# Kernel tuning notes

Hardware: AMD Instinct MI355X
Metric: run time of the kernel (lower is better)

## Reference

```python
import jax, jax.numpy as jnp
import numpy as np

B, T, D = 2, 2048, 1024
H, DH = 16, 64          # num_heads, size_per_head
NU = H * DH             # num_units == 1024


def setup_inputs() -> dict:
    key = jax.random.key(0)
    ks = jax.random.split(key, 8)
    s = 0.02
    return {
        "queries": jax.random.normal(ks[0], (B, T, D), jnp.float32),
        "keys": jax.random.normal(ks[1], (B, T, D), jnp.float32),
        "Wq": jax.random.normal(ks[2], (D, NU), jnp.float32) * s,
        "bq": jnp.zeros((NU,), jnp.float32),
        "Wk": jax.random.normal(ks[3], (D, NU), jnp.float32) * s,
        "bk": jnp.zeros((NU,), jnp.float32),
        "Wv": jax.random.normal(ks[4], (D, NU), jnp.float32) * s,
        "bv": jnp.zeros((NU,), jnp.float32),
    }


def reference(queries, keys, Wq, bq, Wk, bk, Wv, bv):
    # QKV projections
    q = queries @ Wq + bq            # [B, T, NU]
    k = keys @ Wk + bk
    v = keys @ Wv + bv
    # split heads: [B, T, H, DH] -> [B, H, T, DH]
    q_ = q.reshape(B, T, H, DH).transpose(0, 2, 1, 3)
    k_ = k.reshape(B, T, H, DH).transpose(0, 2, 1, 3)
    v_ = v.reshape(B, T, H, DH).transpose(0, 2, 1, 3)
    # scores scaled by num_units**-0.5 (full hidden dim, as in source)
    scores = jnp.einsum("bhqd,bhkd->bhqk", q_, k_) * (NU ** -0.5)
    # causal mask: triu(ones).T == lower-triangular; zeros -> -inf
    causal = jnp.tril(jnp.ones((T, T), bool))
    scores = jnp.where(causal, scores, -jnp.inf)
    weights = jax.nn.softmax(scores, axis=-1)   # [B, H, T, T]
    # dropout is identity in eval/reference
    out = jnp.einsum("bhqk,bhkd->bhqd", weights, v_)  # [B, H, T, DH]
    # merge heads back to [B, T, NU]
    out = out.transpose(0, 2, 1, 3).reshape(B, T, NU)
    return out, weights
```

## Files before the change

### kernel.cpp

```cpp
#include <hip/hip_runtime.h>
#include <cstddef>
#include <cstdint>

namespace {
constexpr int B_ = 2, T_ = 2048, D_ = 1024, H_ = 16, DH_ = 64, NU_ = 1024;
constexpr float SCALE = 0.03125f;
constexpr size_t OUT_ELEMS = (size_t)B_ * T_ * NU_;
}

using f4  = __attribute__((ext_vector_type(4))) float;
using s8v = __attribute__((ext_vector_type(8))) short;
using s4v = __attribute__((ext_vector_type(4))) short;

#define MFMA16(a, b, c) __builtin_amdgcn_mfma_f32_16x16x32_bf16((a), (b), (c), 0, 0, 0)

__device__ __forceinline__ float4 ld4(const float* p) { return *reinterpret_cast<const float4*>(p); }
__device__ __forceinline__ void st4(float* p, const float4 v) { *reinterpret_cast<float4*>(p) = v; }
__device__ __forceinline__ short f2bf(float f) {
    union { float f; uint32_t u; } v{f};
    uint32_t r = (v.u + 0x7fffu + ((v.u >> 16) & 1u)) >> 16;
    return (short)r;
}

#if __has_builtin(__builtin_amdgcn_global_load_lds)
#define HAVE_GLOAD_LDS 1
__device__ __forceinline__ void load_lds16(const void* g, void* l) {
    __builtin_amdgcn_global_load_lds(
        (const __attribute__((address_space(1))) void*)g,
        (__attribute__((address_space(3))) void*)l, 16, 0, 0);
}
#else
#define HAVE_GLOAD_LDS 0
#endif

__global__ __launch_bounds__(256) void cvt_x_kernel(
    const float* __restrict__ q, const float* __restrict__ k,
    short* __restrict__ qx, short* __restrict__ kx)
{
    const float* src = blockIdx.y ? k : q;
    short* dst       = blockIdx.y ? kx : qx;
    size_t i = ((size_t)blockIdx.x * 256 + threadIdx.x) * 8;
    float4 a = ld4(src + i), b = ld4(src + i + 4);
    s8v o = { f2bf(a.x), f2bf(a.y), f2bf(a.z), f2bf(a.w),
              f2bf(b.x), f2bf(b.y), f2bf(b.z), f2bf(b.w) };
    *reinterpret_cast<s8v*>(dst + i) = o;
}

__global__ __launch_bounds__(256) void cvt_w_kernel(
    const float* __restrict__ Wq, const float* __restrict__ Wk,
    const float* __restrict__ Wv, short* __restrict__ wt3)
{
    const int z = blockIdx.z;
    const float* W = (z == 0) ? Wq : (z == 1) ? Wk : Wv;
    short* dst = wt3 + (size_t)z * D_ * NU_;
    const int n0 = blockIdx.x * 64, k0 = blockIdx.y * 64;
    __shared__ float tl[64][68];
    const int rr = threadIdx.x >> 2, cc = (threadIdx.x & 3) * 16;
    const float* s = W + (size_t)(k0 + rr) * NU_ + n0 + cc;
    st4(&tl[rr][cc + 0],  ld4(s + 0));
    st4(&tl[rr][cc + 4],  ld4(s + 4));
    st4(&tl[rr][cc + 8],  ld4(s + 8));
    st4(&tl[rr][cc + 12], ld4(s + 12));
    __syncthreads();
    short* d = dst + (size_t)(n0 + rr) * D_ + k0 + cc;
#pragma unroll
    for (int c = 0; c < 4; ++c) {
        s4v o = { f2bf(tl[cc + c * 4 + 0][rr]), f2bf(tl[cc + c * 4 + 1][rr]),
                  f2bf(tl[cc + c * 4 + 2][rr]), f2bf(tl[cc + c * 4 + 3][rr]) };
        *reinterpret_cast<s4v*>(d + c * 4) = o;
    }
}

__global__ __launch_bounds__(256) void proj_mfma(
    const short* __restrict__ qx, const short* __restrict__ kx,
    const short* __restrict__ wt3,
    const float* __restrict__ bq, const float* __restrict__ bk,
    const float* __restrict__ bv,
    short* __restrict__ qb, short* __restrict__ kb, short* __restrict__ vt)
{
    const int lin = blockIdx.z * 256 + blockIdx.y * 8 + blockIdx.x;
    const int virt = (lin & 7) * 96 + (lin >> 3);
    const int z = virt >> 8, rem = virt & 255;
    const int m0 = (rem >> 3) * 128, n0 = (rem & 7) * 128;

    const short* __restrict__ X  = (z == 0) ? qx : kx;
    const short* __restrict__ Wt = wt3 + (size_t)z * D_ * NU_;
    const float* __restrict__ bias = (z == 0) ? bq : (z == 1) ? bk : bv;

    const int t = threadIdx.x, w = t >> 6, l = t & 63;
    const int lr = l & 15, lg = l >> 4;
    const int wr = w >> 1, wc = w & 1;

    __shared__ short Asl[128 * 64];
    __shared__ short Bsl[128 * 64];

    f4 acc[4][4];
#pragma unroll
    for (int m = 0; m < 4; ++m)
#pragma unroll
        for (int n = 0; n < 4; ++n) acc[m][n] = (f4){0.f, 0.f, 0.f, 0.f};

    for (int k0 = 0; k0 < D_; k0 += 64) {
#if HAVE_GLOAD_LDS
#pragma unroll
        for (int j = 0; j < 4; ++j) {
            const int c0 = (w * 4 + j) * 64;
            const int c  = c0 + l;
            const int row = c >> 3, qo = (c & 7) * 8;
            load_lds16(X  + (size_t)(m0 + row) * D_ + k0 + qo, (char*)Asl + (size_t)c0 * 16);
            load_lds16(Wt + (size_t)(n0 + row) * D_ + k0 + qo, (char*)Bsl + (size_t)c0 * 16);
        }
        __syncthreads();
#else
        {
            const int sr = t >> 1, sc = (t & 1) * 32;
            s8v a0 = *reinterpret_cast<const s8v*>(X  + (size_t)(m0 + sr) * D_ + k0 + sc);
            s8v a1 = *reinterpret_cast<const s8v*>(X  + (size_t)(m0 + sr) * D_ + k0 + sc + 8);
            s8v a2 = *reinterpret_cast<const s8v*>(X  + (size_t)(m0 + sr) * D_ + k0 + sc + 16);
            s8v a3 = *reinterpret_cast<const s8v*>(X  + (size_t)(m0 + sr) * D_ + k0 + sc + 24);
            s8v b0 = *reinterpret_cast<const s8v*>(Wt + (size_t)(n0 + sr) * D_ + k0 + sc);
            s8v b1 = *reinterpret_cast<const s8v*>(Wt + (size_t)(n0 + sr) * D_ + k0 + sc + 8);
            s8v b2 = *reinterpret_cast<const s8v*>(Wt + (size_t)(n0 + sr) * D_ + k0 + sc + 16);
            s8v b3 = *reinterpret_cast<const s8v*>(Wt + (size_t)(n0 + sr) * D_ + k0 + sc + 24);
            __syncthreads();
            *reinterpret_cast<s8v*>(&Asl[sr * 64 + sc])      = a0;
            *reinterpret_cast<s8v*>(&Asl[sr * 64 + sc + 8])  = a1;
            *reinterpret_cast<s8v*>(&Asl[sr * 64 + sc + 16]) = a2;
            *reinterpret_cast<s8v*>(&Asl[sr * 64 + sc + 24]) = a3;
            *reinterpret_cast<s8v*>(&Bsl[sr * 64 + sc])      = b0;
            *reinterpret_cast<s8v*>(&Bsl[sr * 64 + sc + 8])  = b1;
            *reinterpret_cast<s8v*>(&Bsl[sr * 64 + sc + 16]) = b2;
            *reinterpret_cast<s8v*>(&Bsl[sr * 64 + sc + 24]) = b3;
            __syncthreads();
        }
#endif

#pragma unroll
        for (int kk = 0; kk < 2; ++kk) {
            s8v af[4], bf[4];
#pragma unroll
            for (int m = 0; m < 4; ++m)
                af[m] = *reinterpret_cast<const s8v*>(
                    &Asl[(wr * 64 + m * 16 + lr) * 64 + kk * 32 + lg * 8]);
#pragma unroll
            for (int n = 0; n < 4; ++n)
                bf[n] = *reinterpret_cast<const s8v*>(
                    &Bsl[(wc * 64 + n * 16 + lr) * 64 + kk * 32 + lg * 8]);
#pragma unroll
            for (int m = 0; m < 4; ++m)
#pragma unroll
                for (int n = 0; n < 4; ++n)
                    acc[m][n] = MFMA16(af[m], bf[n], acc[m][n]);
        }
        __syncthreads();
    }

    if (z < 2) {
        short* __restrict__ Y = (z == 0) ? qb : kb;
#pragma unroll
        for (int n = 0; n < 4; ++n) {
            const int col = n0 + wc * 64 + n * 16 + lr;
            const float bval = bias[col];
#pragma unroll
            for (int m = 0; m < 4; ++m) {
                const int row0 = m0 + wr * 64 + m * 16 + lg * 4;
#pragma unroll
                for (int r = 0; r < 4; ++r)
                    Y[(size_t)(row0 + r) * NU_ + col] = f2bf(acc[m][n][r] + bval);
            }
        }
    } else {
#pragma unroll
        for (int n = 0; n < 4; ++n) {
            const int col = n0 + wc * 64 + n * 16 + lr;
            const float bval = bias[col];
            const int hh = col >> 6, dd = col & 63;
#pragma unroll
            for (int m = 0; m < 4; ++m) {
                const int Mi = m0 + wr * 64 + m * 16 + lg * 4;
                const int bb = Mi >> 11, t0 = Mi & 2047;
                s4v o = { f2bf(acc[m][n][0] + bval), f2bf(acc[m][n][1] + bval),
                          f2bf(acc[m][n][2] + bval), f2bf(acc[m][n][3] + bval) };
                *reinterpret_cast<s4v*>(vt + ((size_t)(bb * 16 + hh) * 64 + dd) * T_ + t0) = o;
            }
        }
    }
}

__global__ __launch_bounds__(256) void attn_pv_mfma(
    const short* __restrict__ qb, const short* __restrict__ kb,
    const short* __restrict__ vt, float* __restrict__ rsws,
    float* __restrict__ out)
{
    const int lin = blockIdx.x;
    const int xcd = lin & 7, v = lin >> 3;
    const int bh  = xcd * 4 + (v >> 5);
    const int g64 = 31 - (v & 31);
    const int b = bh >> 4, h = bh & 15;
    const int r0 = g64 * 64;
    const int t = threadIdx.x, w = t >> 6, l = t & 63;
    const int lr = l & 15, lg = l >> 4;
    const int tile16 = g64;

    __shared__ __align__(16) char smem[32 * 1024 + 1024];
    short* Pl    = (short*)smem;
    float* OA    = (float*)smem;
    float* rsbuf = (float*)(smem + 32 * 1024);

    const short* qrow0 = qb + (size_t)(b * T_ + r0 + lr) * NU_ + h * DH_ + lg * 8;
    s8v qf[4][2];
#pragma unroll
    for (int d = 0; d < 4; ++d) {
        qf[d][0] = *reinterpret_cast<const s8v*>(qrow0 + (size_t)d * 16 * NU_);
        qf[d][1] = *reinterpret_cast<const s8v*>(qrow0 + (size_t)d * 16 * NU_ + 32);
    }

    f4 acc[4][4];
#pragma unroll
    for (int d = 0; d < 4; ++d)
#pragma unroll
        for (int nt = 0; nt < 4; ++nt) acc[d][nt] = (f4){0.f, 0.f, 0.f, 0.f};
    float rsum[4] = {0.f, 0.f, 0.f, 0.f};
    const f4 zf = (f4){0.f, 0.f, 0.f, 0.f};
    const int sw = (lr & 7) << 3;
    const short* kbase0 = kb + (size_t)(b * T_) * NU_ + h * DH_ + lg * 8;
    short* PlW[4];
#pragma unroll
    for (int d = 0; d < 4; ++d) PlW[d] = &Pl[d * 4096 + w * 1024 + lr * 64];

    for (int ch = w; ch <= tile16; ch += 4) {
        const int jc = ch * 64;
        const bool diag = (ch == tile16);
        const short* kbase = kbase0 + (size_t)jc * NU_;

#pragma unroll
        for (int nt = 0; nt < 4; ++nt) {
            const short* kr = kbase + (size_t)(nt * 16 + lr) * NU_;
            s8v kf0 = *reinterpret_cast<const s8v*>(kr);
            s8v kf1 = *reinterpret_cast<const s8v*>(kr + 32);
            const int jl = nt * 16 + lg * 4;
#pragma unroll
            for (int d = 0; d < 4; ++d) {
                f4 a = MFMA16(kf0, qf[d][0], zf);
                f4 s = MFMA16(kf1, qf[d][1], a);
                float e[4];
#pragma unroll
                for (int r = 0; r < 4; ++r) {
                    float vv = __expf(s[r] * SCALE);
                    if (diag && (jl + r > d * 16 + lr)) vv = 0.f;
                    e[r] = vv;
                }
                rsum[d] += (e[0] + e[1]) + (e[2] + e[3]);
                s4v pv = { f2bf(e[0]), f2bf(e[1]), f2bf(e[2]), f2bf(e[3]) };
                *reinterpret_cast<s4v*>(PlW[d] + (jl ^ sw)) = pv;
            }
        }

        s8v pf[4][2];
#pragma unroll
        for (int d = 0; d < 4; ++d) {
            pf[d][0] = *reinterpret_cast<const s8v*>(PlW[d] + ((lg * 8) ^ sw));
            pf[d][1] = *reinterpret_cast<const s8v*>(PlW[d] + ((32 + lg * 8) ^ sw));
        }
#pragma unroll
        for (int nt = 0; nt < 4; ++nt) {
            const short* vr = vt + (size_t)(bh * 64 + nt * 16 + lr) * T_ + jc + lg * 8;
            s8v vf0 = *reinterpret_cast<const s8v*>(vr);
            s8v vf1 = *reinterpret_cast<const s8v*>(vr + 32);
#pragma unroll
            for (int d = 0; d < 4; ++d) {
                acc[d][nt] = MFMA16(pf[d][0], vf0, acc[d][nt]);
                acc[d][nt] = MFMA16(pf[d][1], vf1, acc[d][nt]);
            }
        }
    }

#pragma unroll
    for (int d = 0; d < 4; ++d) {
        rsum[d] += __shfl_xor(rsum[d], 16);
        rsum[d] += __shfl_xor(rsum[d], 32);
    }

    __syncthreads();
    if (lg == 0) {
#pragma unroll
        for (int d = 0; d < 4; ++d) rsbuf[d * 64 + w * 16 + lr] = rsum[d];
    }

#pragma unroll
    for (int d = 0; d < 4; ++d) {
#pragma unroll
        for (int nt = 0; nt < 4; ++nt)
            st4(&OA[(size_t)(w * 64 + l) * 16 + nt * 4], *(const float4*)&acc[d][nt]);
        __syncthreads();
        float osum[4] = {0.f, 0.f, 0.f, 0.f};
#pragma unroll
        for (int wv = 0; wv < 4; ++wv) {
            float4 p = *(const float4*)&OA[(size_t)(wv * 64 + l) * 16 + w * 4];
#pragma unroll
            for (int r = 0; r < 4; ++r) osum[r] += (&p.x)[r];
        }
#pragma unroll
        for (int r = 0; r < 4; ++r) {
            const int ro = lg * 4 + r;
            const float rt = rsbuf[d * 64 + ro] + rsbuf[d * 64 + 16 + ro]
                           + rsbuf[d * 64 + 32 + ro] + rsbuf[d * 64 + 48 + ro];
            out[(size_t)(b * T_ + r0 + d * 16 + ro) * NU_ + h * DH_ + w * 16 + lr] =
                osum[r] / rt;
        }
        if (w == 0 && t < 16)
            rsws[(size_t)bh * T_ + r0 + d * 16 + t] =
                rsbuf[d * 64 + t] + rsbuf[d * 64 + 16 + t]
                + rsbuf[d * 64 + 32 + t] + rsbuf[d * 64 + 48 + t];
        __syncthreads();
    }
}

__global__ __launch_bounds__(256) void attn_wts_mfma(
    const short* __restrict__ qb, const short* __restrict__ kb,
    const float* __restrict__ rsws, float* __restrict__ wts)
{
    const int lin = blockIdx.x;
    const int xcd = lin & 7, v = lin >> 3;
    const int bh  = xcd * 4 + (v >> 7);
    const int rem = v & 127;
    const int qt2 = 15 - (rem >> 3);
    const int jb  = rem & 7;
    const int b = bh >> 4, h = bh & 15;
    const int r0 = qt2 * 128;
    const int chmax = 2 * qt2 + 1;
    const int t = threadIdx.x, w = t >> 6, l = t & 63;
    const int lr = l & 15, lg = l >> 4;

    const int iA = r0 + w * 16 + lr;
    const int iB = iA + 64;

    const short* qrowA = qb + (size_t)(b * T_ + iA) * NU_ + h * DH_ + lg * 8;
    const s8v qA0 = *reinterpret_cast<const s8v*>(qrowA);
    const s8v qA1 = *reinterpret_cast<const s8v*>(qrowA + 32);
    const s8v qB0 = *reinterpret_cast<const s8v*>(qrowA + 64 * NU_);
    const s8v qB1 = *reinterpret_cast<const s8v*>(qrowA + 64 * NU_ + 32);
    const f4 zf = (f4){0.f, 0.f, 0.f, 0.f};

    const float invA = 1.f / rsws[(size_t)bh * T_ + iA];
    const float invB = 1.f / rsws[(size_t)bh * T_ + iB];
    float* const wrowA = &wts[((size_t)bh * T_ + iA) * T_];
    float* const wrowB = &wts[((size_t)bh * T_ + iB) * T_];
    const short* kbase0 = kb + (size_t)(b * T_) * NU_ + h * DH_ + lg * 8;

#pragma unroll
    for (int cx = 0; cx < 4; ++cx) {
        const int ch = jb * 4 + cx;
        const int jc = ch * 64;
        if (ch <= chmax) {
            const short* kbase = kbase0 + (size_t)jc * NU_;
            f4 sA[4], sB[4];
#pragma unroll
            for (int nt = 0; nt < 4; ++nt) {
                const short* kr = kbase + (size_t)(nt * 16 + lr) * NU_;
                s8v kf0 = *reinterpret_cast<const s8v*>(kr);
                s8v kf1 = *reinterpret_cast<const s8v*>(kr + 32);
                f4 aA = MFMA16(kf0, qA0, zf);
                sA[nt] = MFMA16(kf1, qA1, aA);
                f4 aB = MFMA16(kf0, qB0, zf);
                sB[nt] = MFMA16(kf1, qB1, aB);
            }
#pragma unroll
            for (int nt = 0; nt < 4; ++nt) {
                float4 oA, oB;
                float* eA = &oA.x;
                float* eB = &oB.x;
#pragma unroll
                for (int r = 0; r < 4; ++r) {
                    const int j = jc + nt * 16 + lg * 4 + r;
                    eA[r] = (j <= iA) ? __expf(sA[nt][r] * SCALE) * invA : 0.f;
                    eB[r] = (j <= iB) ? __expf(sB[nt][r] * SCALE) * invB : 0.f;
                }
                st4(wrowA + jc + nt * 16 + lg * 4, oA);
                st4(wrowB + jc + nt * 16 + lg * 4, oB);
            }
        } else {
            const float4 z4 = make_float4(0.f, 0.f, 0.f, 0.f);
#pragma unroll
            for (int half = 0; half < 2; ++half) {
                float* dst = &wts[((size_t)bh * T_ + r0 + half * 64 + (t >> 2)) * T_
                                  + jc + (t & 3) * 16];
                st4(dst + 0, z4); st4(dst + 4, z4);
                st4(dst + 8, z4); st4(dst + 12, z4);
            }
        }
    }
}

extern "C" void kernel_launch(void* const* d_in, const int* in_sizes, int n_in,
                              void* d_out, int out_size, void* d_ws, size_t ws_size,
                              hipStream_t stream)
{
    const float* queries = (const float*)d_in[0];
    const float* keys    = (const float*)d_in[1];
    const float* Wq = (const float*)d_in[2];
    const float* bq = (const float*)d_in[3];
    const float* Wk = (const float*)d_in[4];
    const float* bk = (const float*)d_in[5];
    const float* Wv = (const float*)d_in[6];
    const float* bv = (const float*)d_in[7];

    float* out = (float*)d_out;
    float* wts = out + OUT_ELEMS;

    short* qx = (short*)d_ws;
    short* kx = qx + (size_t)B_ * T_ * D_;
    short* wt = kx + (size_t)B_ * T_ * D_;
    short* qb = wt + (size_t)3 * D_ * NU_;
    short* kb = qb + (size_t)B_ * T_ * NU_;
    short* vt = kb + (size_t)B_ * T_ * NU_;
    float* rsws = (float*)(vt + (size_t)B_ * T_ * NU_);

    cvt_x_kernel<<<dim3((B_ * T_ * D_) / 2048, 2), 256, 0, stream>>>(queries, keys, qx, kx);
    cvt_w_kernel<<<dim3(16, 16, 3), 256, 0, stream>>>(Wq, Wk, Wv, wt);
    proj_mfma<<<dim3(8, 32, 3), 256, 0, stream>>>(
        qx, kx, wt, bq, bk, bv, qb, kb, vt);
    attn_pv_mfma<<<dim3(1024), 256, 0, stream>>>(qb, kb, vt, rsws, out);
    attn_wts_mfma<<<dim3(4096), 256, 0, stream>>>(qb, kb, rsws, wts);
}
```

Baseline: 283.8 us.

## Fuse attention weights output into PV kernel, dropping separate weights kernel

```diff
diff --git a/kernel.cpp b/kernel.cpp
--- a/kernel.cpp
+++ b/kernel.cpp
@@ -187,10 +187,10 @@
     }
 }
 
-__global__ __launch_bounds__(256) void attn_pv_mfma(
+__global__ __launch_bounds__(256) void attn_fused_mfma(
     const short* __restrict__ qb, const short* __restrict__ kb,
-    const short* __restrict__ vt, float* __restrict__ rsws,
-    float* __restrict__ out)
+    const short* __restrict__ vt, float* __restrict__ out,
+    float* __restrict__ wts)
 {
     const int lin = blockIdx.x;
     const int xcd = lin & 7, v = lin >> 3;
@@ -308,85 +308,49 @@
             out[(size_t)(b * T_ + r0 + d * 16 + ro) * NU_ + h * DH_ + w * 16 + lr] =
                 osum[r] / rt;
         }
-        if (w == 0 && t < 16)
-            rsws[(size_t)bh * T_ + r0 + d * 16 + t] =
-                rsbuf[d * 64 + t] + rsbuf[d * 64 + 16 + t]
-                + rsbuf[d * 64 + 32 + t] + rsbuf[d * 64 + 48 + t];
         __syncthreads();
     }
-}
-
-__global__ __launch_bounds__(256) void attn_wts_mfma(
-    const short* __restrict__ qb, const short* __restrict__ kb,
-    const float* __restrict__ rsws, float* __restrict__ wts)
-{
-    const int lin = blockIdx.x;
-    const int xcd = lin & 7, v = lin >> 3;
-    const int bh  = xcd * 4 + (v >> 7);
-    const int rem = v & 127;
-    const int qt2 = 15 - (rem >> 3);
-    const int jb  = rem & 7;
-    const int b = bh >> 4, h = bh & 15;
-    const int r0 = qt2 * 128;
-    const int chmax = 2 * qt2 + 1;
-    const int t = threadIdx.x, w = t >> 6, l = t & 63;
-    const int lr = l & 15, lg = l >> 4;
-
-    const int iA = r0 + w * 16 + lr;
-    const int iB = iA + 64;
-
-    const short* qrowA = qb + (size_t)(b * T_ + iA) * NU_ + h * DH_ + lg * 8;
-    const s8v qA0 = *reinterpret_cast<const s8v*>(qrowA);
-    const s8v qA1 = *reinterpret_cast<const s8v*>(qrowA + 32);
-    const s8v qB0 = *reinterpret_cast<const s8v*>(qrowA + 64 * NU_);
-    const s8v qB1 = *reinterpret_cast<const s8v*>(qrowA + 64 * NU_ + 32);
-    const f4 zf = (f4){0.f, 0.f, 0.f, 0.f};
-
-    const float invA = 1.f / rsws[(size_t)bh * T_ + iA];
-    const float invB = 1.f / rsws[(size_t)bh * T_ + iB];
-    float* const wrowA = &wts[((size_t)bh * T_ + iA) * T_];
-    float* const wrowB = &wts[((size_t)bh * T_ + iB) * T_];
-    const short* kbase0 = kb + (size_t)(b * T_) * NU_ + h * DH_ + lg * 8;
-
-#pragma unroll
-    for (int cx = 0; cx < 4; ++cx) {
-        const int ch = jb * 4 + cx;
+
+    float invd[4];
+#pragma unroll
+    for (int d = 0; d < 4; ++d)
+        invd[d] = 1.f / (rsbuf[d * 64 + lr] + rsbuf[d * 64 + 16 + lr]
+                       + rsbuf[d * 64 + 32 + lr] + rsbuf[d * 64 + 48 + lr]);
+    float* const wbase = &wts[((size_t)bh * T_ + r0 + lr) * T_];
+
+    for (int ch = w; ch < T_ / 64; ch += 4) {
         const int jc = ch * 64;
-        if (ch <= chmax) {
+        if (ch <= tile16) {
+            const bool diag = (ch == tile16);
             const short* kbase = kbase0 + (size_t)jc * NU_;
-            f4 sA[4], sB[4];
 #pragma unroll
             for (int nt = 0; nt < 4; ++nt) {
                 const short* kr = kbase + (size_t)(nt * 16 + lr) * NU_;
                 s8v kf0 = *reinterpret_cast<const s8v*>(kr);
                 s8v kf1 = *reinterpret_cast<const s8v*>(kr + 32);
-                f4 aA = MFMA16(kf0, qA0, zf);
-                sA[nt] = MFMA16(kf1, qA1, aA);
-                f4 aB = MFMA16(kf0, qB0, zf);
-                sB[nt] = MFMA16(kf1, qB1, aB);
-            }
-#pragma unroll
-            for (int nt = 0; nt < 4; ++nt) {
-                float4 oA, oB;
-                float* eA = &oA.x;
-                float* eB = &oB.x;
-#pragma unroll
-                for (int r = 0; r < 4; ++r) {
-                    const int j = jc + nt * 16 + lg * 4 + r;
-                    eA[r] = (j <= iA) ? __expf(sA[nt][r] * SCALE) * invA : 0.f;
-                    eB[r] = (j <= iB) ? __expf(sB[nt][r] * SCALE) * invB : 0.f;
+                const int jl = nt * 16 + lg * 4;
+#pragma unroll
+                for (int d = 0; d < 4; ++d) {
+                    f4 a = MFMA16(kf0, qf[d][0], zf);
+                    f4 s = MFMA16(kf1, qf[d][1], a);
+                    float4 o;
+#pragma unroll
+                    for (int r = 0; r < 4; ++r) {
+                        float vv = __expf(s[r] * SCALE) * invd[d];
+                        if (diag && (jl + r > d * 16 + lr)) vv = 0.f;
+                        (&o.x)[r] = vv;
+                    }
+                    st4(wbase + (size_t)d * 16 * T_ + jc + jl, o);
                 }
-                st4(wrowA + jc + nt * 16 + lg * 4, oA);
-                st4(wrowB + jc + nt * 16 + lg * 4, oB);
             }
         } else {
             const float4 z4 = make_float4(0.f, 0.f, 0.f, 0.f);
 #pragma unroll
-            for (int half = 0; half < 2; ++half) {
-                float* dst = &wts[((size_t)bh * T_ + r0 + half * 64 + (t >> 2)) * T_
-                                  + jc + (t & 3) * 16];
-                st4(dst + 0, z4); st4(dst + 4, z4);
-                st4(dst + 8, z4); st4(dst + 12, z4);
+            for (int nt = 0; nt < 4; ++nt) {
+                const int jl = nt * 16 + lg * 4;
+#pragma unroll
+                for (int d = 0; d < 4; ++d)
+                    st4(wbase + (size_t)d * 16 * T_ + jc + jl, z4);
             }
         }
     }
@@ -414,12 +378,10 @@
     short* qb = wt + (size_t)3 * D_ * NU_;
     short* kb = qb + (size_t)B_ * T_ * NU_;
     short* vt = kb + (size_t)B_ * T_ * NU_;
-    float* rsws = (float*)(vt + (size_t)B_ * T_ * NU_);
 
     cvt_x_kernel<<<dim3((B_ * T_ * D_) / 2048, 2), 256, 0, stream>>>(queries, keys, qx, kx);
     cvt_w_kernel<<<dim3(16, 16, 3), 256, 0, stream>>>(Wq, Wk, Wv, wt);
     proj_mfma<<<dim3(8, 32, 3), 256, 0, stream>>>(
         qx, kx, wt, bq, bk, bv, qb, kb, vt);
-    attn_pv_mfma<<<dim3(1024), 256, 0, stream>>>(qb, kb, vt, rsws, out);
-    attn_wts_mfma<<<dim3(4096), 256, 0, stream>>>(qb, kb, rsws, wts);
-}
+    attn_fused_mfma<<<dim3(1024), 256, 0, stream>>>(qb, kb, vt, out, wts);
+}
```

New measurement: 284.4 us. Within noise of the previous version (+0.2%).

## Move masked-region zero fill of weights into projection kernel launch

Applied to the files above, without the earlier changes.

```diff
diff --git a/kernel.cpp b/kernel.cpp
--- a/kernel.cpp
+++ b/kernel.cpp
@@ -76,9 +76,40 @@
     const short* __restrict__ wt3,
     const float* __restrict__ bq, const float* __restrict__ bk,
     const float* __restrict__ bv,
-    short* __restrict__ qb, short* __restrict__ kb, short* __restrict__ vt)
-{
-    const int lin = blockIdx.z * 256 + blockIdx.y * 8 + blockIdx.x;
+    short* __restrict__ qb, short* __restrict__ kb, short* __restrict__ vt,
+    float* __restrict__ wts)
+{
+    const int bid = blockIdx.x;
+    const int t = threadIdx.x, w = t >> 6, l = t & 63;
+
+    if (bid >= 768) {
+        const int f = bid - 768;
+        const int xcd = f & 7, v = f >> 3;
+        const int bh  = xcd * 4 + (v >> 7);
+        const int rem = v & 127;
+        const int qt2 = 15 - (rem >> 3);
+        const int jb  = rem & 7;
+        const int r0 = qt2 * 128;
+        const int chmax = 2 * qt2 + 1;
+        const float4 z4 = make_float4(0.f, 0.f, 0.f, 0.f);
+#pragma unroll
+        for (int cx = 0; cx < 4; ++cx) {
+            const int ch = jb * 4 + cx;
+            if (ch > chmax) {
+                const int jc = ch * 64;
+#pragma unroll
+                for (int half = 0; half < 2; ++half) {
+                    float* dst = &wts[((size_t)bh * T_ + r0 + half * 64 + (t >> 2)) * T_
+                                      + jc + (t & 3) * 16];
+                    st4(dst + 0, z4); st4(dst + 4, z4);
+                    st4(dst + 8, z4); st4(dst + 12, z4);
+                }
+            }
+        }
+        return;
+    }
+
+    const int lin = bid;
     const int virt = (lin & 7) * 96 + (lin >> 3);
     const int z = virt >> 8, rem = virt & 255;
     const int m0 = (rem >> 3) * 128, n0 = (rem & 7) * 128;
@@ -87,7 +118,6 @@
     const short* __restrict__ Wt = wt3 + (size_t)z * D_ * NU_;
     const float* __restrict__ bias = (z == 0) ? bq : (z == 1) ? bk : bv;
 
-    const int t = threadIdx.x, w = t >> 6, l = t & 63;
     const int lr = l & 15, lg = l >> 4;
     const int wr = w >> 1, wc = w & 1;
 
@@ -326,9 +356,10 @@
     const int rem = v & 127;
     const int qt2 = 15 - (rem >> 3);
     const int jb  = rem & 7;
+    const int chmax = 2 * qt2 + 1;
+    if (jb * 4 > chmax) return;
     const int b = bh >> 4, h = bh & 15;
     const int r0 = qt2 * 128;
-    const int chmax = 2 * qt2 + 1;
     const int t = threadIdx.x, w = t >> 6, l = t & 63;
     const int lr = l & 15, lg = l >> 4;
 
@@ -351,43 +382,33 @@
 #pragma unroll
     for (int cx = 0; cx < 4; ++cx) {
         const int ch = jb * 4 + cx;
+        if (ch > chmax) continue;
         const int jc = ch * 64;
-        if (ch <= chmax) {
-            const short* kbase = kbase0 + (size_t)jc * NU_;
-            f4 sA[4], sB[4];
-#pragma unroll
-            for (int nt = 0; nt < 4; ++nt) {
-                const short* kr = kbase + (size_t)(nt * 16 + lr) * NU_;
-                s8v kf0 = *reinterpret_cast<const s8v*>(kr);
-                s8v kf1 = *reinterpret_cast<const s8v*>(kr + 32);
-                f4 aA = MFMA16(kf0, qA0, zf);
-                sA[nt] = MFMA16(kf1, qA1, aA);
-                f4 aB = MFMA16(kf0, qB0, zf);
-                sB[nt] = MFMA16(kf1, qB1, aB);
-            }
-#pragma unroll
-            for (int nt = 0; nt < 4; ++nt) {
-                float4 oA, oB;
-                float* eA = &oA.x;
-                float* eB = &oB.x;
-#pragma unroll
-                for (int r = 0; r < 4; ++r) {
-                    const int j = jc + nt * 16 + lg * 4 + r;
-                    eA[r] = (j <= iA) ? __expf(sA[nt][r] * SCALE) * invA : 0.f;
-                    eB[r] = (j <= iB) ? __expf(sB[nt][r] * SCALE) * invB : 0.f;
-                }
-                st4(wrowA + jc + nt * 16 + lg * 4, oA);
-                st4(wrowB + jc + nt * 16 + lg * 4, oB);
-            }
-        } else {
-            const float4 z4 = make_float4(0.f, 0.f, 0.f, 0.f);
-#pragma unroll
-            for (int half = 0; half < 2; ++half) {
-                float* dst = &wts[((size_t)bh * T_ + r0 + half * 64 + (t >> 2)) * T_
-                                  + jc + (t & 3) * 16];
-                st4(dst + 0, z4); st4(dst + 4, z4);
-                st4(dst + 8, z4); st4(dst + 12, z4);
-            }
+        const short* kbase = kbase0 + (size_t)jc * NU_;
+        f4 sA[4], sB[4];
+#pragma unroll
+        for (int nt = 0; nt < 4; ++nt) {
+            const short* kr = kbase + (size_t)(nt * 16 + lr) * NU_;
+            s8v kf0 = *reinterpret_cast<const s8v*>(kr);
+            s8v kf1 = *reinterpret_cast<const s8v*>(kr + 32);
+            f4 aA = MFMA16(kf0, qA0, zf);
+            sA[nt] = MFMA16(kf1, qA1, aA);
+            f4 aB = MFMA16(kf0, qB0, zf);
+            sB[nt] = MFMA16(kf1, qB1, aB);
+        }
+#pragma unroll
+        for (int nt = 0; nt < 4; ++nt) {
+            float4 oA, oB;
+            float* eA = &oA.x;
+            float* eB = &oB.x;
+#pragma unroll
+            for (int r = 0; r < 4; ++r) {
+                const int j = jc + nt * 16 + lg * 4 + r;
+                eA[r] = (j <= iA) ? __expf(sA[nt][r] * SCALE) * invA : 0.f;
+                eB[r] = (j <= iB) ? __expf(sB[nt][r] * SCALE) * invB : 0.f;
+            }
+            st4(wrowA + jc + nt * 16 + lg * 4, oA);
+            st4(wrowB + jc + nt * 16 + lg * 4, oB);
         }
     }
 }
@@ -416,10 +437,10 @@
     short* vt = kb + (size_t)B_ * T_ * NU_;
     float* rsws = (float*)(vt + (size_t)B_ * T_ * NU_);
 
-    cvt_x_kernel<<<dim3((B_ * T_ * D_) / 2048, 2), 256, 0, stream>>>(queries, keys, qx, kx);
+    cvt_x_kernel<<<dim3(2048, 2), 256, 0, stream>>>(queries, keys, qx, kx);
     cvt_w_kernel<<<dim3(16, 16, 3), 256, 0, stream>>>(Wq, Wk, Wv, wt);
-    proj_mfma<<<dim3(8, 32, 3), 256, 0, stream>>>(
-        qx, kx, wt, bq, bk, bv, qb, kb, vt);
+    proj_mfma<<<dim3(4864), 256, 0, stream>>>(
+        qx, kx, wt, bq, bk, bv, qb, kb, vt, wts);
     attn_pv_mfma<<<dim3(1024), 256, 0, stream>>>(qb, kb, vt, rsws, out);
     attn_wts_mfma<<<dim3(4096), 256, 0, stream>>>(qb, kb, rsws, wts);
 }
```

Result: slower. 321.1 us (+13.1%).
